# Kernel optimization log

Hardware: AMD Instinct MI355X
Metric: run time of the kernel (lower is better)

Reference implementation:

```python
import jax, jax.numpy as jnp
import numpy as np

N = 300000  # active lattice vertices
K = 9       # permutohedral 1-ring stencil: center + 2*(d+1) neighbors, d=3
F = 64      # nr_filters


def setup_inputs() -> dict:
    key = jax.random.key(0)
    k1, k2, k3, k4 = jax.random.split(key, 4)
    lv = jax.random.normal(k1, (N, F), dtype=jnp.float32)
    neighbors = jax.random.randint(k2, (N, K), 0, N, dtype=jnp.int64)
    # center tap is the vertex itself (tap 0)
    neighbors = neighbors.at[:, 0].set(jnp.arange(N, dtype=jnp.int64))
    scale = 1.0 / np.sqrt(K * F)
    w1 = jax.random.normal(k3, (K, F, F), dtype=jnp.float32) * scale
    w2 = jax.random.normal(k4, (K, F, F), dtype=jnp.float32) * scale
    b1 = jnp.zeros((F,), dtype=jnp.float32)
    b2 = jnp.zeros((F,), dtype=jnp.float32)
    return {"lv": lv, "neighbors": neighbors, "w1": w1, "b1": b1, "w2": w2, "b2": b2}


def _lattice_conv(x, neighbors, w, b):
    # gather neighbor values: [N, K, F], then per-tap matmul and sum over taps
    g = x[neighbors]  # irregular gather
    return jnp.einsum('nkf,kfo->no', g, w) + b


def reference(lv, neighbors, w1, b1, w2, b2):
    identity = lv
    # ReluConv 1: relu -> lattice conv (dropout disabled)
    x = _lattice_conv(jax.nn.relu(lv), neighbors, w1, b1)
    # ReluConv 2: relu -> lattice conv
    x = _lattice_conv(jax.nn.relu(x), neighbors, w2, b2)
    # residual add
    return x + identity
```

## Files before the change

### kernel.cpp

```cpp
#include <hip/hip_runtime.h>

#define NV 300000
#define KT 9
#define NF 64
#define NBLK ((NV + 63) / 64)

typedef __attribute__((ext_vector_type(8))) short bf16x8;
typedef __attribute__((ext_vector_type(4))) float f32x4;
typedef __attribute__((ext_vector_type(4))) float f4;
typedef __attribute__((ext_vector_type(4))) unsigned short u16x4;

__device__ __forceinline__ unsigned short f2bf(float f) {
    union { float f; unsigned int u; } a; a.f = f;
    unsigned int u = a.u;
    return (unsigned short)((u + 0x7FFFu + ((u >> 16) & 1u)) >> 16);
}

__global__ void prep_w_kernel(const float* __restrict__ w1,
                              const float* __restrict__ w2,
                              unsigned short* __restrict__ wt1,
                              unsigned short* __restrict__ wt2) {
    int b = blockIdx.x;
    const float* w = (b < 9) ? w1 : w2;
    unsigned short* wt = (b < 9) ? wt1 : wt2;
    int k = (b < 9) ? b : b - 9;
    for (int e = threadIdx.x; e < NF * NF; e += 256) {
        int o = e >> 6, f = e & 63;
        wt[(k * NF + o) * NF + f] = f2bf(w[(k * NF + f) * NF + o]);
    }
}

__global__ void prep_x_kernel(const float* __restrict__ lv,
                              unsigned short* __restrict__ xbf0) {
    const int n4 = NV * NF / 4;
    int i = blockIdx.x * 256 + threadIdx.x;
    if (i < n4) {
        f4 v = ((const f4*)lv)[i];
        u16x4 r;
        #pragma unroll
        for (int j = 0; j < 4; ++j) r[j] = f2bf(fmaxf(v[j], 0.f));
        ((u16x4*)xbf0)[i] = r;
    }
}

template<int LAYER>
__global__ __launch_bounds__(256, 4)
void conv_kernel(const unsigned short* __restrict__ xin,
                 const int* __restrict__ nbr,
                 const unsigned short* __restrict__ wt,
                 const float* __restrict__ bias,
                 const float* __restrict__ resid,
                 unsigned short* __restrict__ bfout,
                 float* __restrict__ fout)
{
    __shared__ unsigned short gA[4][64][64];
    __shared__ int nbs[576];

    const int tid  = threadIdx.x;
    const int lane = tid & 63;
    const int wv   = tid >> 6;
    const int base = blockIdx.x * 64;

    for (int e = tid; e < 576; e += 256) {
        long ge = (long)base * 9 + e;
        nbs[e] = (ge < (long)NV * 9) ? nbr[ge] : 0;
    }

    const int bcol = wv * 16 + (lane & 15);
    const int bk   = (lane >> 4) * 8;
    bf16x8 bw[KT][2];
    #pragma unroll
    for (int k = 0; k < KT; ++k) {
        #pragma unroll
        for (int kk = 0; kk < 2; ++kk)
            bw[k][kk] = *(const bf16x8*)&wt[(k * 64 + bcol) * 64 + kk * 32 + bk];
    }

    f32x4 acc[4];
    #pragma unroll
    for (int im = 0; im < 4; ++im) acc[im] = (f32x4){0.f, 0.f, 0.f, 0.f};

    __syncthreads();

    const int sr_off = lane >> 3;
    const int sj     = lane & 7;
    auto stage = [&](int k, int buf) {
        #pragma unroll
        for (int h = 0; h < 2; ++h) {
            const int rblk = wv + h * 4;
            const int r    = rblk * 8 + sr_off;
            const int nb   = nbs[r * 9 + k];
            const int gcol = sj ^ (r & 7);
            const unsigned short* src = xin + nb * 64 + gcol * 8;
            __builtin_amdgcn_global_load_lds(
                (const __attribute__((address_space(1))) unsigned int*)src,
                (__attribute__((address_space(3))) unsigned int*)&gA[buf][rblk * 8][0],
                16, 0, 0);
        }
    };

    stage(0, 0); stage(1, 1); stage(2, 2);

    #pragma unroll
    for (int k = 0; k < KT; ++k) {
        if (k <= 6)      asm volatile("s_waitcnt vmcnt(4)" ::: "memory");
        else if (k == 7) asm volatile("s_waitcnt vmcnt(2)" ::: "memory");
        else             asm volatile("s_waitcnt vmcnt(0)" ::: "memory");
        __syncthreads();
        if (k + 3 < KT) stage(k + 3, (k + 3) & 3);

        #pragma unroll
        for (int im = 0; im < 4; ++im) {
            #pragma unroll
            for (int kk = 0; kk < 2; ++kk) {
                const int row  = im * 16 + (lane & 15);
                const int c16  = kk * 4 + (lane >> 4);
                const int swc  = c16 ^ (row & 7);
                bf16x8 a = *(const bf16x8*)&gA[k & 3][row][swc * 8];
                acc[im] = __builtin_amdgcn_mfma_f32_16x16x32_bf16(a, bw[k][kk], acc[im], 0, 0, 0);
            }
        }
    }

    const int ocol = wv * 16 + (lane & 15);
    const int orow = (lane >> 4) * 4;
    const float bv = bias[ocol];
    #pragma unroll
    for (int im = 0; im < 4; ++im) {
        #pragma unroll
        for (int j = 0; j < 4; ++j) {
            const int r = base + im * 16 + orow + j;
            if (r < NV) {
                float v = acc[im][j] + bv;
                if (LAYER == 1) {
                    bfout[r * 64 + ocol] = f2bf(fmaxf(v, 0.f));
                } else {
                    fout[r * 64 + ocol] = v + resid[r * 64 + ocol];
                }
            }
        }
    }
}

extern "C" void kernel_launch(void* const* d_in, const int* in_sizes, int n_in,
                              void* d_out, int out_size, void* d_ws, size_t ws_size,
                              hipStream_t stream) {
    const float* lv  = (const float*)d_in[0];
    const int*   nbr = (const int*)d_in[1];
    const float* w1  = (const float*)d_in[2];
    const float* b1  = (const float*)d_in[3];
    const float* w2  = (const float*)d_in[4];
    const float* b2  = (const float*)d_in[5];
    float* out = (float*)d_out;

    char* ws = (char*)d_ws;
    unsigned short* xbf0 = (unsigned short*)ws;
    unsigned short* xbf1 = (unsigned short*)(ws + 38400000);
    unsigned short* wt1  = (unsigned short*)(ws + 76800000);
    unsigned short* wt2  = (unsigned short*)(ws + 76873728);

    const int n4blk = (NV * NF / 4 + 255) / 256;
    prep_w_kernel<<<18, 256, 0, stream>>>(w1, w2, wt1, wt2);
    prep_x_kernel<<<n4blk, 256, 0, stream>>>(lv, xbf0);
    conv_kernel<1><<<NBLK, 256, 0, stream>>>(xbf0, nbr, wt1, b1, nullptr, xbf1, nullptr);
    conv_kernel<2><<<NBLK, 256, 0, stream>>>(xbf1, nbr, wt2, b2, lv, nullptr, out);
}
```

Baseline: 325.8 us.

## Issue all nine tap gathers up front and merge prep kernels

The conv kernel now gives each of the nine taps its own LDS buffer and issues every neighbor gather at the start. It then waits on decreasing vmcnt values tap by tap, replacing the rolling 4-buffer, 3-deep pipeline. The aim is more memory-level parallelism for the irregular gathers and fewer barriers. The cost is roughly 74KB of LDS per block, with launch bounds lowered to 2 blocks per CU, which reduces occupancy. The weight and input prep kernels are also fused into one launch to save a kernel launch.

```diff
diff --git a/kernel.cpp b/kernel.cpp
--- a/kernel.cpp
+++ b/kernel.cpp
@@ -16,35 +16,36 @@
     return (unsigned short)((u + 0x7FFFu + ((u >> 16) & 1u)) >> 16);
 }
 
-__global__ void prep_w_kernel(const float* __restrict__ w1,
-                              const float* __restrict__ w2,
-                              unsigned short* __restrict__ wt1,
-                              unsigned short* __restrict__ wt2) {
+__global__ void prep_kernel(const float* __restrict__ lv,
+                            const float* __restrict__ w1,
+                            const float* __restrict__ w2,
+                            unsigned short* __restrict__ xbf0,
+                            unsigned short* __restrict__ wt1,
+                            unsigned short* __restrict__ wt2) {
     int b = blockIdx.x;
-    const float* w = (b < 9) ? w1 : w2;
-    unsigned short* wt = (b < 9) ? wt1 : wt2;
-    int k = (b < 9) ? b : b - 9;
-    for (int e = threadIdx.x; e < NF * NF; e += 256) {
-        int o = e >> 6, f = e & 63;
-        wt[(k * NF + o) * NF + f] = f2bf(w[(k * NF + f) * NF + o]);
-    }
-}
-
-__global__ void prep_x_kernel(const float* __restrict__ lv,
-                              unsigned short* __restrict__ xbf0) {
-    const int n4 = NV * NF / 4;
-    int i = blockIdx.x * 256 + threadIdx.x;
-    if (i < n4) {
-        f4 v = ((const f4*)lv)[i];
-        u16x4 r;
-        #pragma unroll
-        for (int j = 0; j < 4; ++j) r[j] = f2bf(fmaxf(v[j], 0.f));
-        ((u16x4*)xbf0)[i] = r;
+    if (b < 18) {
+        const float* w = (b < 9) ? w1 : w2;
+        unsigned short* wt = (b < 9) ? wt1 : wt2;
+        int k = (b < 9) ? b : b - 9;
+        for (int e = threadIdx.x; e < NF * NF; e += 256) {
+            int o = e >> 6, f = e & 63;
+            wt[(k * NF + o) * NF + f] = f2bf(w[(k * NF + f) * NF + o]);
+        }
+    } else {
+        const int n4 = NV * NF / 4;
+        int i = (b - 18) * 256 + threadIdx.x;
+        if (i < n4) {
+            f4 v = ((const f4*)lv)[i];
+            u16x4 r;
+            #pragma unroll
+            for (int j = 0; j < 4; ++j) r[j] = f2bf(fmaxf(v[j], 0.f));
+            ((u16x4*)xbf0)[i] = r;
+        }
     }
 }
 
 template<int LAYER>
-__global__ __launch_bounds__(256, 4)
+__global__ __launch_bounds__(256, 2)
 void conv_kernel(const unsigned short* __restrict__ xin,
                  const int* __restrict__ nbr,
                  const unsigned short* __restrict__ wt,
@@ -53,7 +54,7 @@
                  unsigned short* __restrict__ bfout,
                  float* __restrict__ fout)
 {
-    __shared__ unsigned short gA[4][64][64];
+    __shared__ unsigned short gA[KT][64][64];
     __shared__ int nbs[576];
 
     const int tid  = threadIdx.x;
@@ -84,7 +85,8 @@
 
     const int sr_off = lane >> 3;
     const int sj     = lane & 7;
-    auto stage = [&](int k, int buf) {
+    #pragma unroll
+    for (int k = 0; k < KT; ++k) {
         #pragma unroll
         for (int h = 0; h < 2; ++h) {
             const int rblk = wv + h * 4;
@@ -94,33 +96,32 @@
             const unsigned short* src = xin + nb * 64 + gcol * 8;
             __builtin_amdgcn_global_load_lds(
                 (const __attribute__((address_space(1))) unsigned int*)src,
-                (__attribute__((address_space(3))) unsigned int*)&gA[buf][rblk * 8][0],
+                (__attribute__((address_space(3))) unsigned int*)&gA[k][rblk * 8][0],
                 16, 0, 0);
         }
-    };
+    }
 
-    stage(0, 0); stage(1, 1); stage(2, 2);
-
-    #pragma unroll
-    for (int k = 0; k < KT; ++k) {
-        if (k <= 6)      asm volatile("s_waitcnt vmcnt(4)" ::: "memory");
-        else if (k == 7) asm volatile("s_waitcnt vmcnt(2)" ::: "memory");
-        else             asm volatile("s_waitcnt vmcnt(0)" ::: "memory");
-        __syncthreads();
-        if (k + 3 < KT) stage(k + 3, (k + 3) & 3);
-
+    auto tap = [&](int k) {
         #pragma unroll
         for (int im = 0; im < 4; ++im) {
             #pragma unroll
             for (int kk = 0; kk < 2; ++kk) {
-                const int row  = im * 16 + (lane & 15);
-                const int c16  = kk * 4 + (lane >> 4);
-                const int swc  = c16 ^ (row & 7);
-                bf16x8 a = *(const bf16x8*)&gA[k & 3][row][swc * 8];
+                const int row = im * 16 + (lane & 15);
+                const int c16 = kk * 4 + (lane >> 4);
+                const int swc = c16 ^ (row & 7);
+                bf16x8 a = *(const bf16x8*)&gA[k][row][swc * 8];
                 acc[im] = __builtin_amdgcn_mfma_f32_16x16x32_bf16(a, bw[k][kk], acc[im], 0, 0, 0);
             }
         }
-    }
+    };
+
+    #define PHASE(K, VM)                                              \
+        asm volatile("s_waitcnt vmcnt(" #VM ")" ::: "memory");        \
+        __builtin_amdgcn_s_barrier();                                 \
+        tap(K);
+    PHASE(0, 16) PHASE(1, 14) PHASE(2, 12) PHASE(3, 10) PHASE(4, 8)
+    PHASE(5, 6)  PHASE(6, 4)  PHASE(7, 2)  PHASE(8, 0)
+    #undef PHASE
 
     const int ocol = wv * 16 + (lane & 15);
     const int orow = (lane >> 4) * 4;
@@ -160,8 +161,7 @@
     unsigned short* wt2  = (unsigned short*)(ws + 76873728);
 
     const int n4blk = (NV * NF / 4 + 255) / 256;
-    prep_w_kernel<<<18, 256, 0, stream>>>(w1, w2, wt1, wt2);
-    prep_x_kernel<<<n4blk, 256, 0, stream>>>(lv, xbf0);
+    prep_kernel<<<18 + n4blk, 256, 0, stream>>>(lv, w1, w2, xbf0, wt1, wt2);
     conv_kernel<1><<<NBLK, 256, 0, stream>>>(xbf0, nbr, wt1, b1, nullptr, xbf1, nullptr);
     conv_kernel<2><<<NBLK, 256, 0, stream>>>(xbf1, nbr, wt2, b2, lv, nullptr, out);
 }
```

New measurement: 369.6 us. 13.4% more time.
